# Performance work log

Hardware: AMD Instinct MI355X
Metric: run time of the kernel (lower is better)

## Reference

```python
import jax, jax.numpy as jnp
import numpy as np

N = 50000      # nodes
E = 800000     # edges per view (before self loops)
F_IN = 256     # node feature dim
H = 4          # attention heads
C = 128        # hidden dim (per-head out_channels; concat=False -> mean over heads)
V = 3          # views
NEG_SLOPE = 0.2


def gat_view(x, edge_index, W, a_src, a_dst, b):
    """PyG-style GATConv(heads=H, concat=False) + ELU. Adds self loops."""
    n = x.shape[0]
    loops = jnp.arange(n, dtype=edge_index.dtype)
    src = jnp.concatenate([edge_index[0], loops])  # [E+N]
    dst = jnp.concatenate([edge_index[1], loops])
    h = (x @ W).reshape(n, H, C)                    # [N,H,C]
    s_src = jnp.sum(h * a_src, axis=-1)             # [N,H]
    s_dst = jnp.sum(h * a_dst, axis=-1)             # [N,H]
    e = jax.nn.leaky_relu(s_src[src] + s_dst[dst], NEG_SLOPE)  # [E+N,H]
    # segment softmax over incoming edges of each destination node
    m = jax.ops.segment_max(e, dst, num_segments=n)
    m = jnp.where(jnp.isfinite(m), m, 0.0)
    ex = jnp.exp(e - m[dst])
    denom = jax.ops.segment_sum(ex, dst, num_segments=n)
    alpha = ex / jnp.maximum(denom[dst], 1e-16)     # [E+N,H]
    out = jax.ops.segment_sum(h[src] * alpha[:, :, None], dst, num_segments=n)  # [N,H,C]
    return jax.nn.elu(out.mean(axis=1) + b)         # [N,C]


def setup_inputs() -> dict:
    key = jax.random.key(0)
    ks = jax.random.split(key, 12)
    d = {
        "x": jax.random.normal(ks[0], (N, F_IN), dtype=jnp.float32),
        "edge_index0": jax.random.randint(ks[1], (2, E), 0, N, dtype=jnp.int32),
        "edge_index1": jax.random.randint(ks[2], (2, E), 0, N, dtype=jnp.int32),
        "edge_index2": jax.random.randint(ks[3], (2, E), 0, N, dtype=jnp.int32),
        "W": jax.random.normal(ks[4], (V, F_IN, H * C), dtype=jnp.float32) * 0.05,
        "a_src": jax.random.normal(ks[5], (V, H, C), dtype=jnp.float32) * 0.05,
        "a_dst": jax.random.normal(ks[6], (V, H, C), dtype=jnp.float32) * 0.05,
        "b": jnp.zeros((V, C), dtype=jnp.float32),
        "fus_w": jax.random.normal(ks[7], (C, 1), dtype=jnp.float32) * 0.05,
        "fus_b": jnp.zeros((1,), dtype=jnp.float32),
        "cls_w1": jax.random.normal(ks[8], (C, C // 2), dtype=jnp.float32) * 0.05,
        "cls_b1": jnp.zeros((C // 2,), dtype=jnp.float32),
        "cls_w2": jax.random.normal(ks[9], (C // 2, 2), dtype=jnp.float32) * 0.05,
        "cls_b2": jnp.zeros((2,), dtype=jnp.float32),
    }
    return d


def reference(x, edge_index0, edge_index1, edge_index2, W, a_src, a_dst, b,
              fus_w, fus_b, cls_w1, cls_b1, cls_w2, cls_b2):
    eis = [edge_index0, edge_index1, edge_index2]
    views = [gat_view(x, eis[v], W[v], a_src[v], a_dst[v], b[v]) for v in range(V)]
    stacked = jnp.stack(views, axis=1)                     # [N,V,C]
    scores = jnp.squeeze(stacked @ fus_w, -1) + fus_b      # [N,V]
    weights = jax.nn.softmax(scores, axis=1)               # view attention
    fused = jnp.sum(stacked * weights[..., None], axis=1)  # [N,C]
    hcls = jax.nn.relu(fused @ cls_w1 + cls_b1)            # dropout = identity (eval)
    logits = hcls @ cls_w2 + cls_b2                        # [N,2]
    return logits, weights
```

## Files before the change

### kernel.cpp

```cpp
#include <hip/hip_runtime.h>
#include <math.h>

#define NN 50000
#define EE 800000
#define FIN 256
#define HH 4
#define CC 128
#define HC 512
#define VV 3
#define QMAX 256

#define NB 196
#define SPB 256
#define CAP 4608
#define EPB 8192

typedef __attribute__((ext_vector_type(8))) short short8;
typedef __attribute__((ext_vector_type(4))) float f32x4;
typedef __attribute__((ext_vector_type(2))) float f32x2;

__device__ __forceinline__ float lrelu(float x){ return x > 0.f ? x : 0.2f*x; }

__device__ __forceinline__ unsigned short f2bf(float f){
  unsigned u = __float_as_uint(f);
  u += 0x7fffu + ((u >> 16) & 1);
  return (unsigned short)(u >> 16);
}

__device__ __forceinline__ float wave_sum64(float v){
#pragma unroll
  for (int off = 32; off; off >>= 1) v += __shfl_xor(v, off);
  return v;
}

__device__ __forceinline__ void async16(void* lds, const void* g){
  __builtin_amdgcn_global_load_lds(
      (const __attribute__((address_space(1))) unsigned*)g,
      (__attribute__((address_space(3))) unsigned*)lds, 16, 0, 0);
}

__global__ __launch_bounds__(256) void cast_x(const float* __restrict__ x,
                                              unsigned short* __restrict__ xb){
  int t = blockIdx.x * 256 + threadIdx.x;
  float4 v = *(const float4*)&x[(size_t)t * 4];
  ushort4 o;
  o.x = f2bf(v.x); o.y = f2bf(v.y); o.z = f2bf(v.z); o.w = f2bf(v.w);
  *(ushort4*)&xb[(size_t)t * 4] = o;
}

__global__ __launch_bounds__(256) void prep_w_all(const float* __restrict__ W,
                                                  unsigned short* __restrict__ wp){
  int t = blockIdx.x * 256 + threadIdx.x;
  int v = t >> 17;
  int tl = t & 131071;
  int k = tl >> 9, n = tl & 511;
  wp[(size_t)v * (FIN * HC) + (size_t)(k >> 5) * (HC * 32) + n * 32 + (k & 31)] = f2bf(W[t]);
}

__global__ __launch_bounds__(256) void gemm_mfma_scores(
    const unsigned short* __restrict__ xb, const unsigned short* __restrict__ wp,
    unsigned char* __restrict__ hb,
    const float* __restrict__ a_src_v, const float* __restrict__ a_dst_v,
    float* __restrict__ ssrc, float* __restrict__ sdst){
  __shared__ short As[128 * 32];
  __shared__ short Bs[128 * 32];
  __shared__ float sred[2][128][2];
  int tid = threadIdx.x;
  int wave = tid >> 6, lane = tid & 63;
  int l16 = lane & 15, q = lane >> 4;
  int wr = wave >> 1, wc = wave & 1;
  int head = blockIdx.y;
  int rowBase = blockIdx.x * 128, colBase = head * 128;

  int off0 = wave * 2048 + lane * 16;
  int off1 = off0 + 1024;
  int arow0 = off0 >> 6, akb0 = (off0 & 63) >> 1;
  int arow1 = off1 >> 6, akb1 = (off1 & 63) >> 1;
  size_t ga0 = (size_t)min(rowBase + arow0, NN - 1) * FIN + akb0;
  size_t ga1 = (size_t)min(rowBase + arow1, NN - 1) * FIN + akb1;
  const unsigned short* wpc = wp + (size_t)colBase * 32;

  f32x4 acc[4][4] = {};
  for (int kt = 0; kt < 8; kt++){
    async16((char*)As + wave * 2048,        xb + ga0 + kt * 32);
    async16((char*)As + wave * 2048 + 1024, xb + ga1 + kt * 32);
    async16((char*)Bs + wave * 2048,        wpc + (size_t)kt * (HC * 32) + (off0 >> 1));
    async16((char*)Bs + wave * 2048 + 1024, wpc + (size_t)kt * (HC * 32) + (off1 >> 1));
    __syncthreads();
    short8 af[4], bf[4];
#pragma unroll
    for (int i = 0; i < 4; i++)
      af[i] = *(const short8*)&As[(wr * 64 + i * 16 + l16) * 32 + q * 8];
#pragma unroll
    for (int j = 0; j < 4; j++)
      bf[j] = *(const short8*)&Bs[(wc * 64 + j * 16 + l16) * 32 + q * 8];
#pragma unroll
    for (int i = 0; i < 4; i++)
#pragma unroll
      for (int j = 0; j < 4; j++)
        acc[i][j] = __builtin_amdgcn_mfma_f32_16x16x32_bf16(af[i], bf[j], acc[i][j], 0, 0, 0);
    __syncthreads();
  }
#pragma unroll
  for (int i = 0; i < 4; i++){
#pragma unroll
    for (int r = 0; r < 4; r++){
      int row = rowBase + wr * 64 + i * 16 + q * 4 + r;
      if (row < NN){
        int p01 = __builtin_amdgcn_cvt_pk_fp8_f32(acc[i][0][r], acc[i][1][r], 0, false);
        int p23 = __builtin_amdgcn_cvt_pk_fp8_f32(acc[i][2][r], acc[i][3][r], 0, false);
        size_t rb = (size_t)row * HC + colBase + wc * 64 + l16;
        hb[rb +  0] = (unsigned char)(p01 & 0xff);
        hb[rb + 16] = (unsigned char)((p01 >> 8) & 0xff);
        hb[rb + 32] = (unsigned char)(p23 & 0xff);
        hb[rb + 48] = (unsigned char)((p23 >> 8) & 0xff);
      }
    }
  }
  float asv[4], adv[4];
#pragma unroll
  for (int j = 0; j < 4; j++){
    int c = wc * 64 + j * 16 + l16;
    asv[j] = a_src_v[head * CC + c];
    adv[j] = a_dst_v[head * CC + c];
  }
  float ps[4][4], pd[4][4];
#pragma unroll
  for (int i = 0; i < 4; i++)
#pragma unroll
    for (int r = 0; r < 4; r++){
      float s = 0.f, d = 0.f;
#pragma unroll
      for (int j = 0; j < 4; j++){
        s = fmaf(acc[i][j][r], asv[j], s);
        d = fmaf(acc[i][j][r], adv[j], d);
      }
      ps[i][r] = s; pd[i][r] = d;
    }
#pragma unroll
  for (int off = 1; off < 16; off <<= 1)
#pragma unroll
    for (int i = 0; i < 4; i++)
#pragma unroll
      for (int r = 0; r < 4; r++){
        ps[i][r] += __shfl_xor(ps[i][r], off);
        pd[i][r] += __shfl_xor(pd[i][r], off);
      }
  if (l16 == 0){
#pragma unroll
    for (int i = 0; i < 4; i++)
#pragma unroll
      for (int r = 0; r < 4; r++){
        int rl = wr * 64 + i * 16 + q * 4 + r;
        sred[wc][rl][0] = ps[i][r];
        sred[wc][rl][1] = pd[i][r];
      }
  }
  __syncthreads();
  if (tid < 128){
    int row = rowBase + tid;
    if (row < NN){
      ssrc[row * HH + head] = sred[0][tid][0] + sred[1][tid][0];
      sdst[row * HH + head] = sred[0][tid][1] + sred[1][tid][1];
    }
  }
}

__global__ __launch_bounds__(256) void bucket_scatter(const int* __restrict__ e0,
    const int* __restrict__ e1, const int* __restrict__ e2,
    int* __restrict__ gcur, unsigned* __restrict__ pairs){
  int v = blockIdx.y;
  const int* ei = (v == 0) ? e0 : ((v == 1) ? e1 : e2);
  __shared__ int cnt[NB];
  __shared__ int base[NB];
  int tid = threadIdx.x;
  for (int i = tid; i < NB; i += 256) cnt[i] = 0;
  __syncthreads();
  int estart = blockIdx.x * EPB;
  int eend = min(estart + EPB, EE);
  for (int e = estart + tid; e < eend; e += 256)
    atomicAdd(&cnt[ei[EE + e] >> 8], 1);
  __syncthreads();
  for (int i = tid; i < NB; i += 256){
    int c = cnt[i];
    base[i] = (c > 0) ? atomicAdd(&gcur[v * NB + i], c) : 0;
    cnt[i] = 0;
  }
  __syncthreads();
  for (int e = estart + tid; e < eend; e += 256){
    int s = ei[e], d = ei[EE + e];
    int b = d >> 8;
    int off = base[b] + atomicAdd(&cnt[b], 1);
    if (off < CAP)
      pairs[(size_t)(v * NB + b) * CAP + off] = ((unsigned)(d & 255) << 16) | (unsigned)s;
  }
}

__global__ __launch_bounds__(256) void bucket_scan(const int* __restrict__ gcur,
                                                   int* __restrict__ bbase){
  int v = blockIdx.x;
  __shared__ int wsum[4];
  int tid = threadIdx.x, lane = tid & 63, wv = tid >> 6;
  int val = 0;
  if (tid < NB) val = min(gcur[v * NB + tid], CAP) + min(SPB, NN - tid * SPB);
  int x = val;
#pragma unroll
  for (int off = 1; off < 64; off <<= 1){
    int t = __shfl_up(x, off);
    if (lane >= off) x += t;
  }
  if (lane == 63) wsum[wv] = x;
  __syncthreads();
  int pre = 0;
#pragma unroll
  for (int w = 0; w < 4; w++) if (w < wv) pre += wsum[w];
  if (tid < NB) bbase[v * NB + tid] = pre + x - val;
}

__global__ __launch_bounds__(256) void bucket_csr(const int* __restrict__ gcur,
    const int* __restrict__ bbase, const unsigned* __restrict__ pairs,
    int* __restrict__ rowptr_all, int* __restrict__ colx_all){
  int v = blockIdx.y, b = blockIdx.x;
  int* rowptr = rowptr_all + v * (NN + 1);
  int* colx = colx_all + (size_t)v * (EE + NN);
  __shared__ int hist[SPB];
  __shared__ int wsum[4];
  __shared__ int lcol[CAP + SPB];
  int tid = threadIdx.x, lane = tid & 63, wv = tid >> 6;
  int node0 = b << 8;
  int nvalid = min(SPB, NN - node0);
  int cnt = min(gcur[v * NB + b], CAP);
  int base = bbase[v * NB + b];
  const unsigned* pp = pairs + (size_t)(v * NB + b) * CAP;
  hist[tid] = (tid < nvalid) ? 1 : 0;
  __syncthreads();
  for (int i = tid; i < cnt; i += 256)
    atomicAdd(&hist[pp[i] >> 16], 1);
  __syncthreads();
  int val = hist[tid];
  int x = val;
#pragma unroll
  for (int off = 1; off < 64; off <<= 1){
    int t = __shfl_up(x, off);
    if (lane >= off) x += t;
  }
  if (lane == 63) wsum[wv] = x;
  __syncthreads();
  int pre = 0;
#pragma unroll
  for (int w = 0; w < 4; w++) if (w < wv) pre += wsum[w];
  int excl = pre + x - val;
  __syncthreads();
  hist[tid] = excl + ((tid < nvalid) ? 1 : 0);
  if (tid < nvalid){
    rowptr[node0 + tid] = base + excl;
    lcol[excl] = node0 + tid;
  }
  __syncthreads();
  for (int i = tid; i < cnt; i += 256){
    unsigned p = pp[i];
    int pos = atomicAdd(&hist[p >> 16], 1);
    lcol[pos] = (int)(p & 0xffffu);
  }
  __syncthreads();
  int total = cnt + nvalid;
  for (int i = tid; i < total; i += 256) colx[base + i] = lcol[i];
  if (b == NB - 1 && tid == 0) rowptr[NN] = base + total;
}

__global__ __launch_bounds__(256) void aggregate(const unsigned char* __restrict__ hb,
    const float* __restrict__ ssrc, const float* __restrict__ sdst,
    const int* __restrict__ rowptr, const int* __restrict__ colx,
    float* __restrict__ ex,
    const float* __restrict__ bv, float* __restrict__ voutv){
  __shared__ float se[4][QMAX * 4];
  int wave = threadIdx.x >> 6, lane = threadIdx.x & 63;
  int node = blockIdx.x * 4 + wave;
  int start = rowptr[node], end = rowptr[node + 1];
  int deg = end - start;
  float4 sd = *(const float4*)&sdst[node * HH];
  for (int i = lane; i < deg; i += 64){
    int src = colx[start + i];
    float4 ss = *(const float4*)&ssrc[src * HH];
    float4 e;
    e.x = __expf(lrelu(ss.x + sd.x));
    e.y = __expf(lrelu(ss.y + sd.y));
    e.z = __expf(lrelu(ss.z + sd.z));
    e.w = __expf(lrelu(ss.w + sd.w));
    if (i < QMAX) *(float4*)&se[wave][i * 4] = e;
    else          *(float4*)&ex[(size_t)(start + i) * 4] = e;
  }
  __syncthreads();
  int myh = lane >> 4;
  const float* sew = se[wave];
  float acc[8] = {0.f, 0.f, 0.f, 0.f, 0.f, 0.f, 0.f, 0.f};
  float dsum = 0.f;
  int cpre = (lane < deg) ? colx[start + lane] : 0;
  uint2 h0, h1, h2, h3;
  {
    int i1 = min(1, deg - 1), i2 = min(2, deg - 1), i3 = min(3, deg - 1);
    int s0 = __shfl(cpre, 0), s1 = __shfl(cpre, i1);
    int s2 = __shfl(cpre, i2), s3 = __shfl(cpre, i3);
    h0 = *(const uint2*)&hb[(size_t)s0 * HC + lane * 8];
    h1 = *(const uint2*)&hb[(size_t)s1 * HC + lane * 8];
    h2 = *(const uint2*)&hb[(size_t)s2 * HC + lane * 8];
    h3 = *(const uint2*)&hb[(size_t)s3 * HC + lane * 8];
  }
#define AGG_LOADE(IDX) (((IDX) < QMAX) ? sew[(IDX) * 4 + myh] \
                                       : ex[(size_t)(start + (IDX)) * 4 + myh])
#define AGG_FMA(CH) { \
    f32x2 p0 = __builtin_amdgcn_cvt_pk_f32_fp8(CH.x, false); \
    f32x2 p1 = __builtin_amdgcn_cvt_pk_f32_fp8(CH.x, true); \
    f32x2 p2 = __builtin_amdgcn_cvt_pk_f32_fp8(CH.y, false); \
    f32x2 p3 = __builtin_amdgcn_cvt_pk_f32_fp8(CH.y, true); \
    acc[0] = fmaf(ce, p0[0], acc[0]); \
    acc[1] = fmaf(ce, p0[1], acc[1]); \
    acc[2] = fmaf(ce, p1[0], acc[2]); \
    acc[3] = fmaf(ce, p1[1], acc[3]); \
    acc[4] = fmaf(ce, p2[0], acc[4]); \
    acc[5] = fmaf(ce, p2[1], acc[5]); \
    acc[6] = fmaf(ce, p3[0], acc[6]); \
    acc[7] = fmaf(ce, p3[1], acc[7]); }
#define AGG_STEP(HP, P) { \
    float ce = AGG_LOADE(i + P); \
    int ni = i + 4 + P; \
    uint2 ch = HP; \
    if (ni < deg){ \
      int ns = (ni < 64) ? __shfl(cpre, ni) : colx[start + ni]; \
      HP = *(const uint2*)&hb[(size_t)ns * HC + lane * 8]; \
    } \
    dsum += ce; \
    AGG_FMA(ch) }
#define AGG_TAIL(HP, P) { \
    float ce = AGG_LOADE(i + P); \
    dsum += ce; \
    AGG_FMA(HP) }
  int i = 0;
  for (; i + 4 <= deg; i += 4){
    AGG_STEP(h0, 0)
    AGG_STEP(h1, 1)
    AGG_STEP(h2, 2)
    AGG_STEP(h3, 3)
  }
  int rem = deg - i;
  if (rem > 0) AGG_TAIL(h0, 0)
  if (rem > 1) AGG_TAIL(h1, 1)
  if (rem > 2) AGG_TAIL(h2, 2)
#undef AGG_STEP
#undef AGG_TAIL
#undef AGG_FMA
#undef AGG_LOADE
  float rinv = 0.25f / fmaxf(dsum, 1e-16f);
#pragma unroll
  for (int j = 0; j < 8; j++) acc[j] *= rinv;
#pragma unroll
  for (int off = 16; off < 64; off <<= 1){
#pragma unroll
    for (int j = 0; j < 8; j++) acc[j] += __shfl_xor(acc[j], off);
  }
  if (lane < 16){
    int c0 = lane * 8;
    float o[8];
#pragma unroll
    for (int j = 0; j < 8; j++){
      float vv = acc[j] + bv[c0 + j];
      o[j] = vv > 0.f ? vv : (__expf(vv) - 1.f);
    }
    *(float4*)&voutv[(size_t)node * CC + c0]     = make_float4(o[0], o[1], o[2], o[3]);
    *(float4*)&voutv[(size_t)node * CC + c0 + 4] = make_float4(o[4], o[5], o[6], o[7]);
  }
}

__global__ __launch_bounds__(256) void fuse_classify(const float* __restrict__ vout,
    const float* __restrict__ fw, const float* __restrict__ fb,
    const float* __restrict__ w1, const float* __restrict__ b1,
    const float* __restrict__ w2, const float* __restrict__ b2,
    float* __restrict__ out){
  __shared__ float sw1[CC * 64];
  __shared__ float sfused[4][CC];
  int tid = threadIdx.x;
  for (int i = tid * 4; i < CC * 64; i += 1024)
    *(float4*)&sw1[i] = *(const float4*)&w1[i];
  __syncthreads();
  int wave = tid >> 6, lane = tid & 63;
  int node = blockIdx.x * 4 + wave;
  float2 v0 = *(const float2*)&vout[(size_t)(0 * NN + node) * CC + lane * 2];
  float2 v1 = *(const float2*)&vout[(size_t)(1 * NN + node) * CC + lane * 2];
  float2 v2 = *(const float2*)&vout[(size_t)(2 * NN + node) * CC + lane * 2];
  float fwa = fw[lane * 2], fwb = fw[lane * 2 + 1];
  float s0 = wave_sum64(v0.x * fwa + v0.y * fwb) + fb[0];
  float s1 = wave_sum64(v1.x * fwa + v1.y * fwb) + fb[0];
  float s2 = wave_sum64(v2.x * fwa + v2.y * fwb) + fb[0];
  float mx = fmaxf(s0, fmaxf(s1, s2));
  float e0 = __expf(s0 - mx), e1 = __expf(s1 - mx), e2 = __expf(s2 - mx);
  float rs = 1.f / (e0 + e1 + e2);
  float w0 = e0 * rs, w1v = e1 * rs, w2v = e2 * rs;
  float f0 = w0 * v0.x + w1v * v1.x + w2v * v2.x;
  float f1 = w0 * v0.y + w1v * v1.y + w2v * v2.y;
  sfused[wave][lane * 2]     = f0;
  sfused[wave][lane * 2 + 1] = f1;
  if (lane < 3){
    float wv = (lane == 0) ? w0 : ((lane == 1) ? w1v : w2v);
    out[2 * NN + node * 3 + lane] = wv;
  }
  __syncthreads();
  float hc = b1[lane];
#pragma unroll 8
  for (int c = 0; c < CC; c++)
    hc = fmaf(sfused[wave][c], sw1[c * 64 + lane], hc);
  hc = fmaxf(hc, 0.f);
  float l0 = wave_sum64(hc * w2[lane * 2]);
  float l1 = wave_sum64(hc * w2[lane * 2 + 1]);
  if (lane == 0){
    out[node * 2]     = l0 + b2[0];
    out[node * 2 + 1] = l1 + b2[1];
  }
}

extern "C" void kernel_launch(void* const* d_in, const int* in_sizes, int n_in,
                              void* d_out, int out_size, void* d_ws, size_t ws_size,
                              hipStream_t stream){
  const float* x      = (const float*)d_in[0];
  const int*   e0     = (const int*)d_in[1];
  const int*   e1     = (const int*)d_in[2];
  const int*   e2     = (const int*)d_in[3];
  const float* W      = (const float*)d_in[4];
  const float* a_src  = (const float*)d_in[5];
  const float* a_dst  = (const float*)d_in[6];
  const float* bb     = (const float*)d_in[7];
  const float* fus_w  = (const float*)d_in[8];
  const float* fus_b  = (const float*)d_in[9];
  const float* cls_w1 = (const float*)d_in[10];
  const float* cls_b1 = (const float*)d_in[11];
  const float* cls_w2 = (const float*)d_in[12];
  const float* cls_b2 = (const float*)d_in[13];
  float* out = (float*)d_out;

  unsigned short* xb = (unsigned short*)d_ws;
  unsigned char* hb  = (unsigned char*)(xb + (size_t)NN * FIN);
  unsigned short* wp = (unsigned short*)(hb + (size_t)NN * HC);
  float* ssrc = (float*)(wp + (size_t)VV * FIN * HC);
  float* sdst = ssrc + (size_t)NN * HH;
  float* vout = sdst + (size_t)NN * HH;
  float* ex   = vout + (size_t)VV * NN * CC;
  unsigned* pairs = (unsigned*)(ex + (size_t)(EE + NN) * HH);
  int* gcur   = (int*)(pairs + (size_t)VV * NB * CAP);
  int* bbase  = gcur + VV * NB;
  int* rowptr = bbase + VV * NB;
  int* colx   = rowptr + VV * (NN + 1);

  hipMemsetAsync(gcur, 0, (size_t)VV * NB * sizeof(int), stream);
  cast_x<<<12500, 256, 0, stream>>>(x, xb);
  prep_w_all<<<1536, 256, 0, stream>>>(W, wp);
  dim3 p1grid((EE + EPB - 1) / EPB, 3);
  bucket_scatter<<<p1grid, 256, 0, stream>>>(e0, e1, e2, gcur, pairs);
  bucket_scan<<<3, 256, 0, stream>>>(gcur, bbase);
  dim3 p2grid(NB, 3);
  bucket_csr<<<p2grid, 256, 0, stream>>>(gcur, bbase, pairs, rowptr, colx);

  dim3 ggrid(391, 4);
  for (int v = 0; v < VV; v++){
    gemm_mfma_scores<<<ggrid, 256, 0, stream>>>(
        xb, wp + (size_t)v * FIN * HC, hb,
        a_src + v * HH * CC, a_dst + v * HH * CC, ssrc, sdst);
    aggregate<<<12500, 256, 0, stream>>>(hb, ssrc, sdst,
        rowptr + v * (NN + 1), colx + (size_t)v * (EE + NN), ex,
        bb + v * CC, vout + (size_t)v * NN * CC);
  }
  fuse_classify<<<12500, 256, 0, stream>>>(vout, fus_w, fus_b, cls_w1, cls_b1,
                                           cls_w2, cls_b2, out);
}
```

Baseline: 645.9 us.

## Batch views into single GEMM/aggregate launches, inline edge scores, bf16 view outputs

Launches the GEMM and the aggregation once each for all three views by adding a grid dimension, which needs per-view buffers for h and the scores. The aggregation drops its separate shared-memory pass that precomputed exp scores. It now computes each edge weight inline from ssrc and runs a deeper 8-way prefetch, plus a simple serial fallback for nodes with degree above 64. View outputs are written as bf16 to halve traffic into fuse_classify, at some cost in precision. The larger three-view h buffer raises workspace use, and the fallback path could be slow on high-degree nodes.

```diff
diff --git a/kernel.cpp b/kernel.cpp
--- a/kernel.cpp
+++ b/kernel.cpp
@@ -8,7 +8,6 @@
 #define CC 128
 #define HC 512
 #define VV 3
-#define QMAX 256
 
 #define NB 196
 #define SPB 256
@@ -25,6 +24,9 @@
   unsigned u = __float_as_uint(f);
   u += 0x7fffu + ((u >> 16) & 1);
   return (unsigned short)(u >> 16);
+}
+__device__ __forceinline__ float bf2f(short b){
+  return __uint_as_float(((unsigned)b & 0xffffu) << 16);
 }
 
 __device__ __forceinline__ float wave_sum64(float v){
@@ -58,10 +60,10 @@
 }
 
 __global__ __launch_bounds__(256) void gemm_mfma_scores(
-    const unsigned short* __restrict__ xb, const unsigned short* __restrict__ wp,
-    unsigned char* __restrict__ hb,
-    const float* __restrict__ a_src_v, const float* __restrict__ a_dst_v,
-    float* __restrict__ ssrc, float* __restrict__ sdst){
+    const unsigned short* __restrict__ xb, const unsigned short* __restrict__ wp_all,
+    unsigned char* __restrict__ hb_all,
+    const float* __restrict__ a_src, const float* __restrict__ a_dst,
+    float* __restrict__ ssrc_all, float* __restrict__ sdst_all){
   __shared__ short As[128 * 32];
   __shared__ short Bs[128 * 32];
   __shared__ float sred[2][128][2];
@@ -69,8 +71,15 @@
   int wave = tid >> 6, lane = tid & 63;
   int l16 = lane & 15, q = lane >> 4;
   int wr = wave >> 1, wc = wave & 1;
-  int head = blockIdx.y;
+  int head = blockIdx.y, v = blockIdx.z;
   int rowBase = blockIdx.x * 128, colBase = head * 128;
+
+  const unsigned short* wp = wp_all + (size_t)v * FIN * HC;
+  unsigned char* hb = hb_all + (size_t)v * NN * HC;
+  const float* a_src_v = a_src + v * HH * CC;
+  const float* a_dst_v = a_dst + v * HH * CC;
+  float* ssrc = ssrc_all + (size_t)v * NN * HH;
+  float* sdst = sdst_all + (size_t)v * NN * HH;
 
   int off0 = wave * 2048 + lane * 16;
   int off1 = off0 + 1024;
@@ -268,88 +277,89 @@
   if (b == NB - 1 && tid == 0) rowptr[NN] = base + total;
 }
 
-__global__ __launch_bounds__(256) void aggregate(const unsigned char* __restrict__ hb,
-    const float* __restrict__ ssrc, const float* __restrict__ sdst,
-    const int* __restrict__ rowptr, const int* __restrict__ colx,
-    float* __restrict__ ex,
-    const float* __restrict__ bv, float* __restrict__ voutv){
-  __shared__ float se[4][QMAX * 4];
+__global__ __launch_bounds__(256) void aggregate(const unsigned char* __restrict__ hb_all,
+    const float* __restrict__ ssrc_all, const float* __restrict__ sdst_all,
+    const int* __restrict__ rowptr_all, const int* __restrict__ colx_all,
+    const float* __restrict__ bb, unsigned short* __restrict__ vout_all){
+  int v = blockIdx.y;
+  const unsigned char* hb = hb_all + (size_t)v * NN * HC;
+  const float* ssrc = ssrc_all + (size_t)v * NN * HH;
+  const float* sdst = sdst_all + (size_t)v * NN * HH;
+  const int* rowptr = rowptr_all + v * (NN + 1);
+  const int* colx = colx_all + (size_t)v * (EE + NN);
+  const float* bv = bb + v * CC;
+  unsigned short* voutv = vout_all + (size_t)v * NN * CC;
+
   int wave = threadIdx.x >> 6, lane = threadIdx.x & 63;
   int node = blockIdx.x * 4 + wave;
-  int start = rowptr[node], end = rowptr[node + 1];
-  int deg = end - start;
-  float4 sd = *(const float4*)&sdst[node * HH];
-  for (int i = lane; i < deg; i += 64){
-    int src = colx[start + i];
-    float4 ss = *(const float4*)&ssrc[src * HH];
-    float4 e;
-    e.x = __expf(lrelu(ss.x + sd.x));
-    e.y = __expf(lrelu(ss.y + sd.y));
-    e.z = __expf(lrelu(ss.z + sd.z));
-    e.w = __expf(lrelu(ss.w + sd.w));
-    if (i < QMAX) *(float4*)&se[wave][i * 4] = e;
-    else          *(float4*)&ex[(size_t)(start + i) * 4] = e;
-  }
-  __syncthreads();
+  int start = rowptr[node];
+  int deg = rowptr[node + 1] - start;
   int myh = lane >> 4;
-  const float* sew = se[wave];
+  float sdh = sdst[node * HH + myh];
   float acc[8] = {0.f, 0.f, 0.f, 0.f, 0.f, 0.f, 0.f, 0.f};
   float dsum = 0.f;
-  int cpre = (lane < deg) ? colx[start + lane] : 0;
-  uint2 h0, h1, h2, h3;
-  {
-    int i1 = min(1, deg - 1), i2 = min(2, deg - 1), i3 = min(3, deg - 1);
-    int s0 = __shfl(cpre, 0), s1 = __shfl(cpre, i1);
-    int s2 = __shfl(cpre, i2), s3 = __shfl(cpre, i3);
-    h0 = *(const uint2*)&hb[(size_t)s0 * HC + lane * 8];
-    h1 = *(const uint2*)&hb[(size_t)s1 * HC + lane * 8];
-    h2 = *(const uint2*)&hb[(size_t)s2 * HC + lane * 8];
-    h3 = *(const uint2*)&hb[(size_t)s3 * HC + lane * 8];
-  }
-#define AGG_LOADE(IDX) (((IDX) < QMAX) ? sew[(IDX) * 4 + myh] \
-                                       : ex[(size_t)(start + (IDX)) * 4 + myh])
-#define AGG_FMA(CH) { \
+
+#define AGG_FMA(CH, CE) { \
     f32x2 p0 = __builtin_amdgcn_cvt_pk_f32_fp8(CH.x, false); \
     f32x2 p1 = __builtin_amdgcn_cvt_pk_f32_fp8(CH.x, true); \
     f32x2 p2 = __builtin_amdgcn_cvt_pk_f32_fp8(CH.y, false); \
     f32x2 p3 = __builtin_amdgcn_cvt_pk_f32_fp8(CH.y, true); \
-    acc[0] = fmaf(ce, p0[0], acc[0]); \
-    acc[1] = fmaf(ce, p0[1], acc[1]); \
-    acc[2] = fmaf(ce, p1[0], acc[2]); \
-    acc[3] = fmaf(ce, p1[1], acc[3]); \
-    acc[4] = fmaf(ce, p2[0], acc[4]); \
-    acc[5] = fmaf(ce, p2[1], acc[5]); \
-    acc[6] = fmaf(ce, p3[0], acc[6]); \
-    acc[7] = fmaf(ce, p3[1], acc[7]); }
-#define AGG_STEP(HP, P) { \
-    float ce = AGG_LOADE(i + P); \
-    int ni = i + 4 + P; \
+    acc[0] = fmaf(CE, p0[0], acc[0]); \
+    acc[1] = fmaf(CE, p0[1], acc[1]); \
+    acc[2] = fmaf(CE, p1[0], acc[2]); \
+    acc[3] = fmaf(CE, p1[1], acc[3]); \
+    acc[4] = fmaf(CE, p2[0], acc[4]); \
+    acc[5] = fmaf(CE, p2[1], acc[5]); \
+    acc[6] = fmaf(CE, p3[0], acc[6]); \
+    acc[7] = fmaf(CE, p3[1], acc[7]); }
+
+  if (deg <= 64){
+    int cpre = (lane < deg) ? colx[start + lane] : 0;
+    uint2 h0, h1, h2, h3, h4, h5, h6, h7;
+    float s0, s1, s2, s3, s4, s5, s6, s7;
+#define AGG_PRO(HP, SP, P) { \
+    int sp = __shfl(cpre, min(P, deg - 1)); \
+    HP = *(const uint2*)&hb[(size_t)(unsigned)(sp * HC) + lane * 8]; \
+    SP = ssrc[sp * HH + myh]; }
+    AGG_PRO(h0, s0, 0) AGG_PRO(h1, s1, 1) AGG_PRO(h2, s2, 2) AGG_PRO(h3, s3, 3)
+    AGG_PRO(h4, s4, 4) AGG_PRO(h5, s5, 5) AGG_PRO(h6, s6, 6) AGG_PRO(h7, s7, 7)
+#undef AGG_PRO
+#define AGG_STEP(HP, SP, P) { \
+    float ce = __expf(lrelu(SP + sdh)); \
+    dsum += ce; \
     uint2 ch = HP; \
+    int ni = i + 8 + P; \
     if (ni < deg){ \
-      int ns = (ni < 64) ? __shfl(cpre, ni) : colx[start + ni]; \
-      HP = *(const uint2*)&hb[(size_t)ns * HC + lane * 8]; \
+      int ns = __shfl(cpre, ni); \
+      HP = *(const uint2*)&hb[(size_t)(unsigned)(ns * HC) + lane * 8]; \
+      SP = ssrc[ns * HH + myh]; \
     } \
+    AGG_FMA(ch, ce) }
+    int i = 0;
+    for (; i + 8 <= deg; i += 8){
+      AGG_STEP(h0, s0, 0) AGG_STEP(h1, s1, 1) AGG_STEP(h2, s2, 2) AGG_STEP(h3, s3, 3)
+      AGG_STEP(h4, s4, 4) AGG_STEP(h5, s5, 5) AGG_STEP(h6, s6, 6) AGG_STEP(h7, s7, 7)
+    }
+#undef AGG_STEP
+    int rem = deg - i;
+#define AGG_TAIL(HP, SP, P) if (rem > P){ \
+    float ce = __expf(lrelu(SP + sdh)); \
     dsum += ce; \
-    AGG_FMA(ch) }
-#define AGG_TAIL(HP, P) { \
-    float ce = AGG_LOADE(i + P); \
-    dsum += ce; \
-    AGG_FMA(HP) }
-  int i = 0;
-  for (; i + 4 <= deg; i += 4){
-    AGG_STEP(h0, 0)
-    AGG_STEP(h1, 1)
-    AGG_STEP(h2, 2)
-    AGG_STEP(h3, 3)
-  }
-  int rem = deg - i;
-  if (rem > 0) AGG_TAIL(h0, 0)
-  if (rem > 1) AGG_TAIL(h1, 1)
-  if (rem > 2) AGG_TAIL(h2, 2)
-#undef AGG_STEP
+    AGG_FMA(HP, ce) }
+    AGG_TAIL(h0, s0, 0) AGG_TAIL(h1, s1, 1) AGG_TAIL(h2, s2, 2) AGG_TAIL(h3, s3, 3)
+    AGG_TAIL(h4, s4, 4) AGG_TAIL(h5, s5, 5) AGG_TAIL(h6, s6, 6)
 #undef AGG_TAIL
+  } else {
+    for (int i = 0; i < deg; i++){
+      int src = colx[start + i];
+      float sv = ssrc[src * HH + myh];
+      float ce = __expf(lrelu(sv + sdh));
+      dsum += ce;
+      uint2 ch = *(const uint2*)&hb[(size_t)(unsigned)(src * HC) + lane * 8];
+      AGG_FMA(ch, ce)
+    }
+  }
 #undef AGG_FMA
-#undef AGG_LOADE
   float rinv = 0.25f / fmaxf(dsum, 1e-16f);
 #pragma unroll
   for (int j = 0; j < 8; j++) acc[j] *= rinv;
@@ -360,18 +370,18 @@
   }
   if (lane < 16){
     int c0 = lane * 8;
-    float o[8];
+    short8 o;
 #pragma unroll
     for (int j = 0; j < 8; j++){
       float vv = acc[j] + bv[c0 + j];
-      o[j] = vv > 0.f ? vv : (__expf(vv) - 1.f);
-    }
-    *(float4*)&voutv[(size_t)node * CC + c0]     = make_float4(o[0], o[1], o[2], o[3]);
-    *(float4*)&voutv[(size_t)node * CC + c0 + 4] = make_float4(o[4], o[5], o[6], o[7]);
-  }
-}
-
-__global__ __launch_bounds__(256) void fuse_classify(const float* __restrict__ vout,
+      float e = vv > 0.f ? vv : (__expf(vv) - 1.f);
+      o[j] = (short)f2bf(e);
+    }
+    *(short8*)&voutv[(size_t)node * CC + c0] = o;
+  }
+}
+
+__global__ __launch_bounds__(256) void fuse_classify(const unsigned short* __restrict__ vb,
     const float* __restrict__ fw, const float* __restrict__ fb,
     const float* __restrict__ w1, const float* __restrict__ b1,
     const float* __restrict__ w2, const float* __restrict__ b2,
@@ -384,19 +394,22 @@
   __syncthreads();
   int wave = tid >> 6, lane = tid & 63;
   int node = blockIdx.x * 4 + wave;
-  float2 v0 = *(const float2*)&vout[(size_t)(0 * NN + node) * CC + lane * 2];
-  float2 v1 = *(const float2*)&vout[(size_t)(1 * NN + node) * CC + lane * 2];
-  float2 v2 = *(const float2*)&vout[(size_t)(2 * NN + node) * CC + lane * 2];
+  unsigned r0 = *(const unsigned*)&vb[(size_t)(0 * NN + node) * CC + lane * 2];
+  unsigned r1 = *(const unsigned*)&vb[(size_t)(1 * NN + node) * CC + lane * 2];
+  unsigned r2 = *(const unsigned*)&vb[(size_t)(2 * NN + node) * CC + lane * 2];
+  float v0x = bf2f((short)(r0 & 0xffffu)), v0y = bf2f((short)(r0 >> 16));
+  float v1x = bf2f((short)(r1 & 0xffffu)), v1y = bf2f((short)(r1 >> 16));
+  float v2x = bf2f((short)(r2 & 0xffffu)), v2y = bf2f((short)(r2 >> 16));
   float fwa = fw[lane * 2], fwb = fw[lane * 2 + 1];
-  float s0 = wave_sum64(v0.x * fwa + v0.y * fwb) + fb[0];
-  float s1 = wave_sum64(v1.x * fwa + v1.y * fwb) + fb[0];
-  float s2 = wave_sum64(v2.x * fwa + v2.y * fwb) + fb[0];
+  float s0 = wave_sum64(v0x * fwa + v0y * fwb) + fb[0];
+  float s1 = wave_sum64(v1x * fwa + v1y * fwb) + fb[0];
+  float s2 = wave_sum64(v2x * fwa + v2y * fwb) + fb[0];
   float mx = fmaxf(s0, fmaxf(s1, s2));
   float e0 = __expf(s0 - mx), e1 = __expf(s1 - mx), e2 = __expf(s2 - mx);
   float rs = 1.f / (e0 + e1 + e2);
   float w0 = e0 * rs, w1v = e1 * rs, w2v = e2 * rs;
-  float f0 = w0 * v0.x + w1v * v1.x + w2v * v2.x;
-  float f1 = w0 * v0.y + w1v * v1.y + w2v * v2.y;
+  float f0 = w0 * v0x + w1v * v1x + w2v * v2x;
+  float f1 = w0 * v0y + w1v * v1y + w2v * v2y;
   sfused[wave][lane * 2]     = f0;
   sfused[wave][lane * 2 + 1] = f1;
   if (lane < 3){
@@ -438,16 +451,15 @@
 
   unsigned short* xb = (unsigned short*)d_ws;
   unsigned char* hb  = (unsigned char*)(xb + (size_t)NN * FIN);
-  unsigned short* wp = (unsigned short*)(hb + (size_t)NN * HC);
+  unsigned short* wp = (unsigned short*)(hb + (size_t)VV * NN * HC);
   float* ssrc = (float*)(wp + (size_t)VV * FIN * HC);
-  float* sdst = ssrc + (size_t)NN * HH;
-  float* vout = sdst + (size_t)NN * HH;
-  float* ex   = vout + (size_t)VV * NN * CC;
-  unsigned* pairs = (unsigned*)(ex + (size_t)(EE + NN) * HH);
-  int* gcur   = (int*)(pairs + (size_t)VV * NB * CAP);
+  float* sdst = ssrc + (size_t)VV * NN * HH;
+  int* gcur   = (int*)(sdst + (size_t)VV * NN * HH);
   int* bbase  = gcur + VV * NB;
   int* rowptr = bbase + VV * NB;
   int* colx   = rowptr + VV * (NN + 1);
+  unsigned* pairs = (unsigned*)(colx + (size_t)VV * (EE + NN));
+  unsigned short* voutb = (unsigned short*)pairs;
 
   hipMemsetAsync(gcur, 0, (size_t)VV * NB * sizeof(int), stream);
   cast_x<<<12500, 256, 0, stream>>>(x, xb);
@@ -458,15 +470,10 @@
   dim3 p2grid(NB, 3);
   bucket_csr<<<p2grid, 256, 0, stream>>>(gcur, bbase, pairs, rowptr, colx);
 
-  dim3 ggrid(391, 4);
-  for (int v = 0; v < VV; v++){
-    gemm_mfma_scores<<<ggrid, 256, 0, stream>>>(
-        xb, wp + (size_t)v * FIN * HC, hb,
-        a_src + v * HH * CC, a_dst + v * HH * CC, ssrc, sdst);
-    aggregate<<<12500, 256, 0, stream>>>(hb, ssrc, sdst,
-        rowptr + v * (NN + 1), colx + (size_t)v * (EE + NN), ex,
-        bb + v * CC, vout + (size_t)v * NN * CC);
-  }
-  fuse_classify<<<12500, 256, 0, stream>>>(vout, fus_w, fus_b, cls_w1, cls_b1,
+  dim3 ggrid(391, 4, 3);
+  gemm_mfma_scores<<<ggrid, 256, 0, stream>>>(xb, wp, hb, a_src, a_dst, ssrc, sdst);
+  dim3 agrid(12500, 3);
+  aggregate<<<agrid, 256, 0, stream>>>(hb, ssrc, sdst, rowptr, colx, bb, voutb);
+  fuse_classify<<<12500, 256, 0, stream>>>(voutb, fus_w, fus_b, cls_w1, cls_b1,
                                            cls_w2, cls_b2, out);
 }
```

After: 545.4 us. 1.18x faster.
